# Performance work log

Hardware: AMD Instinct MI355X
Metric: run time of the kernel (lower is better)

Reference implementation:

```python
import jax, jax.numpy as jnp
import numpy as np

T = 16384   # sequence length
D = 14      # input_size
H = 32      # hidden_dim
M = 4       # number of parallel LSTMs: [main, f1, f2, f3]


def setup_inputs() -> dict:
    key = jax.random.key(0)
    ks = jax.random.split(key, 12)
    s = 1.0 / np.sqrt(H)
    return {
        "x": jax.random.normal(ks[0], (M, T, D), jnp.float32),
        # stacked LSTM params, torch gate order (i, f, g, o)
        "W_ih": jax.random.uniform(ks[1], (M, 4 * H, D), jnp.float32, -s, s),
        "W_hh": jax.random.uniform(ks[2], (M, 4 * H, H), jnp.float32, -s, s),
        "b_ih": jax.random.uniform(ks[3], (M, 4 * H), jnp.float32, -s, s),
        "b_hh": jax.random.uniform(ks[4], (M, 4 * H), jnp.float32, -s, s),
        "Wt": jax.random.uniform(ks[5], (1, 4 * H), jnp.float32, -s, s),
        "bt": jax.random.uniform(ks[6], (1,), jnp.float32, -s, s),
        "Wf1": jax.random.uniform(ks[7], (1, H), jnp.float32, -s, s),
        "bf1": jax.random.uniform(ks[8], (1,), jnp.float32, -s, s),
        "Wf2": jax.random.uniform(ks[9], (1, H), jnp.float32, -s, s),
        "bf2": jax.random.uniform(ks[10], (1,), jnp.float32, -s, s),
    }


def _lstm_last_h(x, W_ih, W_hh, b_ih, b_hh):
    # x: [M, T, D] -> final hidden state h: [M, H] after running all 4
    # single-layer LSTMs in lockstep over the full sequence.
    xT = jnp.swapaxes(x, 0, 1)  # [T, M, D]
    h0 = jnp.zeros((x.shape[0], H), x.dtype)
    c0 = jnp.zeros((x.shape[0], H), x.dtype)

    def step(carry, x_t):
        h, c = carry
        gates = (jnp.einsum('mgd,md->mg', W_ih, x_t) + b_ih
                 + jnp.einsum('mgh,mh->mg', W_hh, h) + b_hh)  # [M, 4H]
        i, f, g, o = jnp.split(gates, 4, axis=-1)
        c = jax.nn.sigmoid(f) * c + jax.nn.sigmoid(i) * jnp.tanh(g)
        h = jax.nn.sigmoid(o) * jnp.tanh(c)
        return (h, c), None

    (h, _), _ = jax.lax.scan(step, (h0, c0), xT)
    return h  # [M, H]


def reference(x, W_ih, W_hh, b_ih, b_hh, Wt, bt, Wf1, bf1, Wf2, bf2):
    h = _lstm_last_h(x, W_ih, W_hh, b_ih, b_hh)  # [4, H]; rows: main, f1, f2, f3
    target_in = h.reshape(1, 4 * H)              # cat(main, f1, f2, f3)
    target_out = target_in @ Wt.T + bt           # [1, 1]
    f1_out = (h[1:2] @ Wf1.T + bf1).reshape(1, 1, 1)
    f2_out = (h[2:3] @ Wf2.T + bf2).reshape(1, 1, 1)
    # original code reuses featureLayer2 for f3 (bug preserved)
    f3_out = (h[3:4] @ Wf2.T + bf2).reshape(1, 1, 1)
    return (target_out, f1_out, f2_out, f3_out)
```

## Files before the change

### kernel.cpp

```cpp
#include <hip/hip_runtime.h>

typedef float v2f __attribute__((ext_vector_type(2)));

#define D_IN 14
#define HID  32

#define LOG2E      1.4426950408889634f
#define TWO_LOG2E  2.8853900817779268f

__device__ __forceinline__ float rcpf(float x) { return __builtin_amdgcn_rcpf(x); }

#if __has_builtin(__builtin_amdgcn_exp2f)
__device__ __forceinline__ float exp2ff(float x) { return __builtin_amdgcn_exp2f(x); }
#else
__device__ __forceinline__ float exp2ff(float x) { return exp2f(x); }
#endif

template<int CTRL>
__device__ __forceinline__ float dppf(float x) {
    return __int_as_float(__builtin_amdgcn_mov_dpp(
        __float_as_int(x), CTRL, 0xf, 0xf, true));
}

__device__ __forceinline__ float xchg32(float x) {
    float a = x, b;
    asm("v_mov_b32 %0, %1" : "=&v"(b) : "v"(x));
    asm("v_permlane32_swap_b32 %0, %1" : "+v"(a), "+v"(b));
    return (a + b) - x;
}
__device__ __forceinline__ float xchg16(float x) {
    float a = x, b;
    asm("v_mov_b32 %0, %1" : "=&v"(b) : "v"(x));
    asm("v_permlane16_swap_b32 %0, %1" : "+v"(a), "+v"(b));
    return (a + b) - x;
}

__global__ __launch_bounds__(64, 1)
void lstm_scan_m(const float* __restrict__ x,
                 const float* __restrict__ W_ih,
                 const float* __restrict__ W_hh,
                 const float* __restrict__ b_ih,
                 const float* __restrict__ b_hh,
                 const float* __restrict__ Wt,  const float* __restrict__ bt,
                 const float* __restrict__ Wf1, const float* __restrict__ bf1,
                 const float* __restrict__ Wf2, const float* __restrict__ bf2,
                 float* __restrict__ hws,
                 unsigned* __restrict__ flag,
                 float* __restrict__ out,
                 int T)
{
    const int m    = blockIdx.x;
    const int lane = threadIdx.x;
    const int hi   = lane >> 5;
    const int j    = lane & 31;
    const int rA   = lane;
    const int rB   = lane + 64;

    const float sA = -LOG2E;
    const float sB = hi ? -LOG2E : TWO_LOG2E;

    int d0;
    {
        int p = __builtin_amdgcn_mov_dpp(lane, 0x121, 0xf, 0xf, true);
        d0 = __builtin_amdgcn_readfirstlane(p);
    }
    const int j16 = j & 16, j15 = j & 15;
    int kk[16];
    #pragma unroll
    for (int s = 0; s < 16; ++s) kk[s] = j16 | ((j15 + s * d0) & 15);

    const float* WOA = W_hh + (size_t)(m * 128 + rA) * HID;
    const float* WOB = W_hh + (size_t)(m * 128 + rB) * HID;
    const float* WPA = W_hh + (size_t)(m * 128 + (rA ^ 16)) * HID;
    const float* WPB = W_hh + (size_t)(m * 128 + (rB ^ 16)) * HID;
    v2f wOA[8], wOB[8], wPA[8], wPB[8];
    #pragma unroll
    for (int q = 0; q < 8; ++q) {
        wOA[q] = (v2f){WOA[kk[2*q]] * sA, WOA[kk[2*q+1]] * sA};
        wOB[q] = (v2f){WOB[kk[2*q]] * sB, WOB[kk[2*q+1]] * sB};
        wPA[q] = (v2f){WPA[kk[2*q]] * sA, WPA[kk[2*q+1]] * sA};
        wPB[q] = (v2f){WPB[kk[2*q]] * sB, WPB[kk[2*q+1]] * sB};
    }

    v2f wax[7], wbx[7];
    {
        const v2f* pA = (const v2f*)(W_ih + (size_t)(m * 128 + rA) * D_IN);
        const v2f* pB = (const v2f*)(W_ih + (size_t)(m * 128 + rB) * D_IN);
        #pragma unroll
        for (int q = 0; q < 7; ++q) {
            v2f a = pA[q], b = pB[q];
            a.x *= sA; a.y *= sA; b.x *= sB; b.y *= sB;
            wax[q] = a; wbx[q] = b;
        }
    }
    const float bA = (b_ih[m * 128 + rA] + b_hh[m * 128 + rA]) * sA;
    const float bB = (b_ih[m * 128 + rB] + b_hh[m * 128 + rB]) * sB;

    const v2f* xs = (const v2f*)(x + (size_t)m * T * D_IN);
    v2f xb0[7], xb1[7];
    #pragma unroll
    for (int q = 0; q < 7; ++q) { xb0[q] = xs[q]; xb1[q] = xs[7 + q]; }

    float c  = 0.0f;
    float vh = 0.0f;

#define STEP(t, xb)                                                            \
    {                                                                          \
                        \
        float g1 = dppf<0x121>(vh), g2 = dppf<0x122>(vh);                      \
        float g3 = dppf<0x123>(vh), g4 = dppf<0x124>(vh);                      \
        float g5 = dppf<0x125>(vh), g6 = dppf<0x126>(vh);                      \
        float g7 = dppf<0x127>(vh), g8 = dppf<0x128>(vh);                      \
        float g9 = dppf<0x129>(vh), gA = dppf<0x12A>(vh);                      \
        float gB = dppf<0x12B>(vh), gC = dppf<0x12C>(vh);                      \
        float gD = dppf<0x12D>(vh), gE = dppf<0x12E>(vh);                      \
        float gF = dppf<0x12F>(vh);                                            \
        v2f hv[8];                                                             \
        hv[0] = (v2f){vh, g1}; hv[1] = (v2f){g2, g3};                          \
        hv[2] = (v2f){g4, g5}; hv[3] = (v2f){g6, g7};                          \
        hv[4] = (v2f){g8, g9}; hv[5] = (v2f){gA, gB};                          \
        hv[6] = (v2f){gC, gD}; hv[7] = (v2f){gE, gF};                          \
                                 \
        v2f av = {bA, 0.0f}, bv = {bB, 0.0f};                                  \
        _Pragma("unroll")                                                      \
        for (int q = 0; q < 7; ++q) {                                          \
            av = __builtin_elementwise_fma(wax[q], xb[q], av);                 \
            bv = __builtin_elementwise_fma(wbx[q], xb[q], bv);                 \
        }                                                                      \
        {                                                                      \
            int tn = (t) + 2; tn = (tn < T) ? tn : (T - 1);                    \
            const v2f* p = xs + (size_t)tn * 7;                                \
            _Pragma("unroll")                                                  \
            for (int q = 0; q < 7; ++q) xb[q] = p[q];                          \
        }                                                                      \
                  \
        v2f oa0 = av, oa1 = {0.0f, 0.0f}, ob0 = bv, ob1 = {0.0f, 0.0f};        \
        v2f pa0 = {0.0f, 0.0f}, pa1 = {0.0f, 0.0f};                            \
        v2f pb0 = {0.0f, 0.0f}, pb1 = {0.0f, 0.0f};                            \
        _Pragma("unroll")                                                      \
        for (int q = 0; q < 8; q += 2) {                                       \
            oa0 = __builtin_elementwise_fma(wOA[q],     hv[q],     oa0);       \
            oa1 = __builtin_elementwise_fma(wOA[q + 1], hv[q + 1], oa1);       \
            ob0 = __builtin_elementwise_fma(wOB[q],     hv[q],     ob0);       \
            ob1 = __builtin_elementwise_fma(wOB[q + 1], hv[q + 1], ob1);       \
            pa0 = __builtin_elementwise_fma(wPA[q],     hv[q],     pa0);       \
            pa1 = __builtin_elementwise_fma(wPA[q + 1], hv[q + 1], pa1);       \
            pb0 = __builtin_elementwise_fma(wPB[q],     hv[q],     pb0);       \
            pb1 = __builtin_elementwise_fma(wPB[q + 1], hv[q + 1], pb1);       \
        }                                                                      \
        v2f oas = oa0 + oa1, obs = ob0 + ob1;                                  \
        v2f pas = pa0 + pa1, pbs = pb0 + pb1;                                  \
        float qa = pas.x + pas.y, qb = pbs.x + pbs.y;                          \
        float ra = xchg16(qa), rb = xchg16(qb);             \
        float accA = (oas.x + oas.y) + ra;                                     \
        float accB = (obs.x + obs.y) + rb;                                     \
                                            \
        float actA = rcpf(1.0f + exp2ff(accA));             \
        float rBv  = rcpf(1.0f + exp2ff(accB));                                \
        float actB = hi ? rBv : __builtin_fmaf(-2.0f, rBv, 1.0f);              \
        float x0   = hi ? actA : actA * actB;                  \
        float y0   = xchg32(x0);                               \
        float y1   = xchg32(actB);                         \
        float sf   = hi ? actA : y0;                                           \
        float u    = hi ? y0   : x0;                                           \
        c = __builtin_fmaf(sf, c, u);                                          \
        float so = hi ? actB : y1;                                             \
        float r2 = rcpf(1.0f + exp2ff(c * TWO_LOG2E));                         \
        float tc = __builtin_fmaf(-2.0f, r2, 1.0f);                            \
        vh = so * tc;                               \
    }

    for (int t = 0; t < T; t += 2) {
        STEP(t, xb0)
        STEP(t + 1, xb1)
    }
#undef STEP

    if (hi) hws[m * 32 + j] = vh;
    __threadfence();

    if (lane == 0) {
        unsigned old = atomicAdd(flag, 1u);
        if (old == 3u) {
            __threadfence();
            float s0 = bt[0];
            #pragma unroll
            for (int k = 0; k < 128; ++k) s0 += hws[k] * Wt[k];
            out[0] = s0;
            float s1 = bf1[0];
            #pragma unroll
            for (int k = 0; k < 32; ++k) s1 += hws[32 + k] * Wf1[k];
            out[1] = s1;
            float s2 = bf2[0];
            #pragma unroll
            for (int k = 0; k < 32; ++k) s2 += hws[64 + k] * Wf2[k];
            out[2] = s2;
            float s3 = bf2[0];
            #pragma unroll
            for (int k = 0; k < 32; ++k) s3 += hws[96 + k] * Wf2[k];
            out[3] = s3;
        }
    }
}

extern "C" void kernel_launch(void* const* d_in, const int* in_sizes, int n_in,
                              void* d_out, int out_size, void* d_ws, size_t ws_size,
                              hipStream_t stream) {
    const float* x    = (const float*)d_in[0];
    const float* W_ih = (const float*)d_in[1];
    const float* W_hh = (const float*)d_in[2];
    const float* b_ih = (const float*)d_in[3];
    const float* b_hh = (const float*)d_in[4];
    const float* Wt   = (const float*)d_in[5];
    const float* bt   = (const float*)d_in[6];
    const float* Wf1  = (const float*)d_in[7];
    const float* bf1  = (const float*)d_in[8];
    const float* Wf2  = (const float*)d_in[9];
    const float* bf2  = (const float*)d_in[10];

    const int T = in_sizes[0] / (4 * D_IN);

    unsigned* flag = (unsigned*)d_ws;
    float*    hws  = (float*)((char*)d_ws + 256);

    hipMemsetAsync(d_ws, 0, 256, stream);

    lstm_scan_m<<<4, 64, 0, stream>>>(x, W_ih, W_hh, b_ih, b_hh,
                                      Wt, bt, Wf1, bf1, Wf2, bf2,
                                      hws, flag, (float*)d_out, T);
}
```

Baseline: 4.524 ms.

## Precompute input projections in a parallel kernel and stream them into the scan

Moves the W_ih·x + bias projection out of the sequential recurrence into a separate parallel kernel that writes pre-scaled gate inputs to workspace. The scan kernel then loads one float4 per step with an 8-step-deep prefetch, which removes 14 FMAs and 7 loads per step from the critical path. The sequence is chunked to fit the workspace, with h and c carried between chunks, and the output heads move to a final kernel. This adds extra launches, workspace traffic and a serial split if the workspace is small.

```diff
diff --git a/kernel.cpp b/kernel.cpp
--- a/kernel.cpp
+++ b/kernel.cpp
@@ -1,9 +1,11 @@
 #include <hip/hip_runtime.h>
 
 typedef float v2f __attribute__((ext_vector_type(2)));
+typedef float v4f __attribute__((ext_vector_type(4)));
 
 #define D_IN 14
 #define HID  32
+#define XT   16
 
 #define LOG2E      1.4426950408889634f
 #define TWO_LOG2E  2.8853900817779268f
@@ -35,19 +37,46 @@
     return (a + b) - x;
 }
 
+__global__ __launch_bounds__(128)
+void xproj_kernel(const float* __restrict__ x,
+                  const float* __restrict__ W_ih,
+                  const float* __restrict__ b_ih,
+                  const float* __restrict__ b_hh,
+                  float* __restrict__ xp,
+                  int t0, int cT, int T)
+{
+    const int m = blockIdx.y;
+    const int r = threadIdx.x;
+    const int tlo = blockIdx.x * XT;
+
+    const float sc = (r < 64) ? -LOG2E : ((r < 96) ? TWO_LOG2E : -LOG2E);
+
+    v2f w[7];
+    const v2f* wp = (const v2f*)(W_ih + (size_t)(m * 128 + r) * D_IN);
+    #pragma unroll
+    for (int q = 0; q < 7; ++q) {
+        v2f t = wp[q]; t.x *= sc; t.y *= sc; w[q] = t;
+    }
+    const float bs = (b_ih[m * 128 + r] + b_hh[m * 128 + r]) * sc;
+
+    #pragma unroll
+    for (int tt = 0; tt < XT; ++tt) {
+        int t = tlo + tt;
+        if (t >= cT) break;
+        const v2f* xr = (const v2f*)(x + ((size_t)m * T + t0 + t) * D_IN);
+        v2f acc = {bs, 0.0f};
+        #pragma unroll
+        for (int q = 0; q < 7; ++q) acc = __builtin_elementwise_fma(w[q], xr[q], acc);
+        float* dst = xp + (((size_t)t * 4 + m) * 64 + (r & 63)) * 4 + (r >> 6) * 2;
+        *(v2f*)dst = acc;
+    }
+}
+
 __global__ __launch_bounds__(64, 1)
-void lstm_scan_m(const float* __restrict__ x,
-                 const float* __restrict__ W_ih,
+void lstm_scan_m(const float* __restrict__ xp,
                  const float* __restrict__ W_hh,
-                 const float* __restrict__ b_ih,
-                 const float* __restrict__ b_hh,
-                 const float* __restrict__ Wt,  const float* __restrict__ bt,
-                 const float* __restrict__ Wf1, const float* __restrict__ bf1,
-                 const float* __restrict__ Wf2, const float* __restrict__ bf2,
-                 float* __restrict__ hws,
-                 unsigned* __restrict__ flag,
-                 float* __restrict__ out,
-                 int T)
+                 float* __restrict__ carry,
+                 int cT, int first)
 {
     const int m    = blockIdx.x;
     const int lane = threadIdx.x;
@@ -82,29 +111,26 @@
         wPB[q] = (v2f){WPB[kk[2*q]] * sB, WPB[kk[2*q+1]] * sB};
     }
 
-    v2f wax[7], wbx[7];
+    const v4f* xpv = (const v4f*)xp + (size_t)m * 64 + lane;
+
+    float c, vh;
+    if (first) { c = 0.0f; vh = 0.0f; }
+    else       { vh = carry[m * 32 + j]; c = carry[128 + m * 32 + j]; }
+
+    v4f s0, s1, s2, s3, s4, s5, s6, s7;
     {
-        const v2f* pA = (const v2f*)(W_ih + (size_t)(m * 128 + rA) * D_IN);
-        const v2f* pB = (const v2f*)(W_ih + (size_t)(m * 128 + rB) * D_IN);
-        #pragma unroll
-        for (int q = 0; q < 7; ++q) {
-            v2f a = pA[q], b = pB[q];
-            a.x *= sA; a.y *= sA; b.x *= sB; b.y *= sB;
-            wax[q] = a; wbx[q] = b;
-        }
-    }
-    const float bA = (b_ih[m * 128 + rA] + b_hh[m * 128 + rA]) * sA;
-    const float bB = (b_ih[m * 128 + rB] + b_hh[m * 128 + rB]) * sB;
-
-    const v2f* xs = (const v2f*)(x + (size_t)m * T * D_IN);
-    v2f xb0[7], xb1[7];
-    #pragma unroll
-    for (int q = 0; q < 7; ++q) { xb0[q] = xs[q]; xb1[q] = xs[7 + q]; }
-
-    float c  = 0.0f;
-    float vh = 0.0f;
-
-#define STEP(t, xb)                                                            \
+        int e = cT - 1;
+        s0 = xpv[(size_t)((0 < e) ? 0 : e) * 256];
+        s1 = xpv[(size_t)((1 < e) ? 1 : e) * 256];
+        s2 = xpv[(size_t)((2 < e) ? 2 : e) * 256];
+        s3 = xpv[(size_t)((3 < e) ? 3 : e) * 256];
+        s4 = xpv[(size_t)((4 < e) ? 4 : e) * 256];
+        s5 = xpv[(size_t)((5 < e) ? 5 : e) * 256];
+        s6 = xpv[(size_t)((6 < e) ? 6 : e) * 256];
+        s7 = xpv[(size_t)((7 < e) ? 7 : e) * 256];
+    }
+
+#define STEP(t, X)                                                             \
     {                                                                          \
                         \
         float g1 = dppf<0x121>(vh), g2 = dppf<0x122>(vh);                      \
@@ -120,21 +146,9 @@
         hv[2] = (v2f){g4, g5}; hv[3] = (v2f){g6, g7};                          \
         hv[4] = (v2f){g8, g9}; hv[5] = (v2f){gA, gB};                          \
         hv[6] = (v2f){gC, gD}; hv[7] = (v2f){gE, gF};                          \
-                                 \
-        v2f av = {bA, 0.0f}, bv = {bB, 0.0f};                                  \
-        _Pragma("unroll")                                                      \
-        for (int q = 0; q < 7; ++q) {                                          \
-            av = __builtin_elementwise_fma(wax[q], xb[q], av);                 \
-            bv = __builtin_elementwise_fma(wbx[q], xb[q], bv);                 \
-        }                                                                      \
-        {                                                                      \
-            int tn = (t) + 2; tn = (tn < T) ? tn : (T - 1);                    \
-            const v2f* p = xs + (size_t)tn * 7;                                \
-            _Pragma("unroll")                                                  \
-            for (int q = 0; q < 7; ++q) xb[q] = p[q];                          \
-        }                                                                      \
-                  \
-        v2f oa0 = av, oa1 = {0.0f, 0.0f}, ob0 = bv, ob1 = {0.0f, 0.0f};        \
+            \
+        v2f oa0 = (v2f){X.x, X.y}, oa1 = {0.0f, 0.0f};                         \
+        v2f ob0 = (v2f){X.z, X.w}, ob1 = {0.0f, 0.0f};                         \
         v2f pa0 = {0.0f, 0.0f}, pa1 = {0.0f, 0.0f};                            \
         v2f pb0 = {0.0f, 0.0f}, pb1 = {0.0f, 0.0f};                            \
         _Pragma("unroll")                                                      \
@@ -148,13 +162,17 @@
             pb0 = __builtin_elementwise_fma(wPB[q],     hv[q],     pb0);       \
             pb1 = __builtin_elementwise_fma(wPB[q + 1], hv[q + 1], pb1);       \
         }                                                                      \
+                          \
+        {                                                                      \
+            int tn = (t) + 8; tn = (tn < cT) ? tn : (cT - 1);                  \
+            X = xpv[(size_t)tn * 256];                                         \
+        }                                                                      \
         v2f oas = oa0 + oa1, obs = ob0 + ob1;                                  \
         v2f pas = pa0 + pa1, pbs = pb0 + pb1;                                  \
         float qa = pas.x + pas.y, qb = pbs.x + pbs.y;                          \
         float ra = xchg16(qa), rb = xchg16(qb);             \
         float accA = (oas.x + oas.y) + ra;                                     \
         float accB = (obs.x + obs.y) + rb;                                     \
-                                            \
         float actA = rcpf(1.0f + exp2ff(accA));             \
         float rBv  = rcpf(1.0f + exp2ff(accB));                                \
         float actB = hi ? rBv : __builtin_fmaf(-2.0f, rBv, 1.0f);              \
@@ -170,36 +188,57 @@
         vh = so * tc;                               \
     }
 
-    for (int t = 0; t < T; t += 2) {
-        STEP(t, xb0)
-        STEP(t + 1, xb1)
+    int t = 0;
+    for (; t + 8 <= cT; t += 8) {
+        STEP(t,     s0)
+        STEP(t + 1, s1)
+        STEP(t + 2, s2)
+        STEP(t + 3, s3)
+        STEP(t + 4, s4)
+        STEP(t + 5, s5)
+        STEP(t + 6, s6)
+        STEP(t + 7, s7)
+    }
+    for (; t < cT; ++t) {
+        v4f q4 = xpv[(size_t)t * 256];
+        STEP(t, q4)
     }
 #undef STEP
 
-    if (hi) hws[m * 32 + j] = vh;
-    __threadfence();
-
-    if (lane == 0) {
-        unsigned old = atomicAdd(flag, 1u);
-        if (old == 3u) {
-            __threadfence();
-            float s0 = bt[0];
-            #pragma unroll
-            for (int k = 0; k < 128; ++k) s0 += hws[k] * Wt[k];
-            out[0] = s0;
-            float s1 = bf1[0];
-            #pragma unroll
-            for (int k = 0; k < 32; ++k) s1 += hws[32 + k] * Wf1[k];
-            out[1] = s1;
-            float s2 = bf2[0];
-            #pragma unroll
-            for (int k = 0; k < 32; ++k) s2 += hws[64 + k] * Wf2[k];
-            out[2] = s2;
-            float s3 = bf2[0];
-            #pragma unroll
-            for (int k = 0; k < 32; ++k) s3 += hws[96 + k] * Wf2[k];
-            out[3] = s3;
-        }
+    if (hi) {
+        carry[m * 32 + j]       = vh;
+        carry[128 + m * 32 + j] = c;
+    }
+}
+
+__global__ __launch_bounds__(64)
+void heads_kernel(const float* __restrict__ carry,
+                  const float* __restrict__ Wt,  const float* __restrict__ bt,
+                  const float* __restrict__ Wf1, const float* __restrict__ bf1,
+                  const float* __restrict__ Wf2, const float* __restrict__ bf2,
+                  float* __restrict__ out)
+{
+    const int tid = threadIdx.x;
+    if (tid == 0) {
+        float s = bt[0];
+        #pragma unroll
+        for (int k = 0; k < 128; ++k) s += carry[k] * Wt[k];
+        out[0] = s;
+    } else if (tid == 1) {
+        float s = bf1[0];
+        #pragma unroll
+        for (int k = 0; k < 32; ++k) s += carry[32 + k] * Wf1[k];
+        out[1] = s;
+    } else if (tid == 2) {
+        float s = bf2[0];
+        #pragma unroll
+        for (int k = 0; k < 32; ++k) s += carry[64 + k] * Wf2[k];
+        out[2] = s;
+    } else if (tid == 3) {
+        float s = bf2[0];
+        #pragma unroll
+        for (int k = 0; k < 32; ++k) s += carry[96 + k] * Wf2[k];
+        out[3] = s;
     }
 }
 
@@ -220,12 +259,30 @@
 
     const int T = in_sizes[0] / (4 * D_IN);
 
-    unsigned* flag = (unsigned*)d_ws;
-    float*    hws  = (float*)((char*)d_ws + 256);
-
-    hipMemsetAsync(d_ws, 0, 256, stream);
-
-    lstm_scan_m<<<4, 64, 0, stream>>>(x, W_ih, W_hh, b_ih, b_hh,
-                                      Wt, bt, Wf1, bf1, Wf2, bf2,
-                                      hws, flag, (float*)d_out, T);
-}
+    float* carry = (float*)d_ws;
+    float* xpbuf = (float*)((char*)d_ws + 1024);
+    size_t avail = (ws_size > 1024) ? ws_size - 1024 : 0;
+
+    long cmax = (long)(avail / 4096);
+    cmax = (cmax / 8) * 8;
+    if (cmax > T) cmax = T;
+    if (cmax < 8) cmax = 8;
+
+    int nch = (T + (int)cmax - 1) / (int)cmax;
+    int cT0 = (T + nch - 1) / nch;
+    cT0 = ((cT0 + 7) / 8) * 8;
+    if (cT0 > (int)cmax) cT0 = (int)cmax;
+
+    int done = 0;
+    while (done < T) {
+        int cT = (T - done < cT0) ? (T - done) : cT0;
+        dim3 gx((cT + XT - 1) / XT, 4);
+        xproj_kernel<<<gx, 128, 0, stream>>>(x, W_ih, b_ih, b_hh, xpbuf,
+                                             done, cT, T);
+        lstm_scan_m<<<4, 64, 0, stream>>>(xpbuf, W_hh, carry,
+                                          cT, done == 0 ? 1 : 0);
+        done += cT;
+    }
+    heads_kernel<<<1, 64, 0, stream>>>(carry, Wt, bt, Wf1, bf1, Wf2, bf2,
+                                       (float*)d_out);
+}
```

New measurement: 3.673 ms (median of 2 runs). 1.23x faster.
